# Kernel tuning notes

Hardware: AMD Instinct MI355X
Metric: run time of the kernel (lower is better)

## Reference

```python
import jax, jax.numpy as jnp
import numpy as np

B, L, H = 2, 1024, 1024   # batch, seq_len, hidden_size
NH, D, K = 16, 64, 4      # num_heads, head_dim, conv kernel
HD = NH * D


def setup_inputs() -> dict:
    key = jax.random.key(0)
    ks = jax.random.split(key, 12)
    s = 0.02  # LeCun-ish init scale as in the torch module
    return {
        "hidden_states": jax.random.normal(ks[0], (B, L, H), jnp.float32),
        "Wq": jax.random.normal(ks[1], (HD, H), jnp.float32) * s,
        "bq": jnp.zeros((HD,), jnp.float32),
        "Wk": jax.random.normal(ks[2], (HD, H), jnp.float32) * s,
        "bk": jnp.zeros((HD,), jnp.float32),
        "Wv": jax.random.normal(ks[3], (HD, H), jnp.float32) * s,
        "bv": jnp.zeros((HD,), jnp.float32),
        "Wa": jax.random.normal(ks[4], (NH, H), jnp.float32) * s,
        "Wb": jax.random.normal(ks[5], (NH, H), jnp.float32) * s,
        "Wconv": jax.random.normal(ks[6], (HD, 1, K), jnp.float32) * s,
        "Wo": jax.random.normal(ks[7], (H, HD), jnp.float32) * s,
        "bo": jnp.zeros((H,), jnp.float32),
    }


def _gated_delta(q, k, v, alpha, beta):
    # q,k,v: [B,L,NH,D]; alpha,beta: [B,L,NH]
    # S_t = S_{t-1} @ (alpha_t * (I - beta_t k_t k_t^T)) + beta_t v_t k_t^T ; o_t = S_t q_t
    eye = jnp.eye(q.shape[-1], dtype=q.dtype)

    def step(S, xs):
        q_t, k_t, v_t, a_t, b_t = xs  # [B,NH,D], [B,NH]
        kk = jnp.einsum('bhd,bhe->bhde', k_t, k_t)
        decay = a_t[..., None, None] * (eye - b_t[..., None, None] * kk)
        S = jnp.einsum('bhde,bhef->bhdf', S, decay) \
            + b_t[..., None, None] * jnp.einsum('bhd,bhe->bhde', v_t, k_t)
        o_t = jnp.einsum('bhde,bhe->bhd', S, q_t)
        return S, o_t

    xs = (jnp.moveaxis(q, 1, 0), jnp.moveaxis(k, 1, 0), jnp.moveaxis(v, 1, 0),
          jnp.moveaxis(alpha, 1, 0), jnp.moveaxis(beta, 1, 0))
    S0 = jnp.zeros((q.shape[0], q.shape[2], q.shape[3], q.shape[3]), q.dtype)
    _, outs = jax.lax.scan(step, S0, xs)  # [L,B,NH,D]
    return jnp.transpose(outs, (1, 2, 0, 3))  # [B,NH,L,D] (matches torch stack+transposes)


def reference(hidden_states, Wq, bq, Wk, bk, Wv, bv, Wa, Wb, Wconv, Wo, bo):
    Bc, Lc, Hc = hidden_states.shape
    q = (hidden_states @ Wq.T + bq).reshape(Bc, Lc, NH, D)
    k = (hidden_states @ Wk.T + bk).reshape(Bc, Lc, NH, D)
    v = (hidden_states @ Wv.T + bv).reshape(Bc, Lc, NH, D)
    alpha = jax.nn.sigmoid(hidden_states @ Wa.T)   # [B,L,NH]
    beta = jax.nn.softplus(hidden_states @ Wb.T)   # [B,L,NH]

    out = _gated_delta(q, k, v, alpha, beta)       # [B,NH,L,D]
    out = out.reshape(Bc, Lc, NH * D)              # replicates torch's reshape of [B,NH,L,D]
    x = jnp.transpose(out, (0, 2, 1))              # [B,HD,L]
    conv = jax.lax.conv_general_dilated(
        x, Wconv, window_strides=(1,), padding=[(K - 1, 0)],
        feature_group_count=NH * D, dimension_numbers=('NCH', 'OIH', 'NCH'))
    x = x + conv                                   # residual depthwise causal conv
    x = jnp.transpose(x, (0, 2, 1))                # [B,L,HD]
    return x @ Wo.T + bo                           # [B,L,H]; dropout is identity at eval
```

## Files before the change

kernel.cpp:

```cpp
#include <hip/hip_runtime.h>
#include <math.h>

#define BB 2
#define LL 1024
#define HH 1024
#define NH 16
#define DD 64
#define HD (NH * DD)
#define MM (BB * LL)
#define RCT 32
#define KEXT 3072
#define NBK 1088

typedef _Float16 f16x8 __attribute__((ext_vector_type(8)));
typedef _Float16 f16x4 __attribute__((ext_vector_type(4)));
typedef float f32x4 __attribute__((ext_vector_type(4)));

__device__ __forceinline__ void load_lds16(const void* g, void* l) {
    __builtin_amdgcn_global_load_lds(
        (const __attribute__((address_space(1))) void*)g,
        (__attribute__((address_space(3))) void*)l, 16, 0, 0);
}

__global__ __launch_bounds__(256) void convert_front(
    const float* __restrict__ hs,
    const float* __restrict__ Wq, const float* __restrict__ Wk,
    const float* __restrict__ Wv, const float* __restrict__ Wa,
    const float* __restrict__ Wb, const float* __restrict__ Wo,
    _Float16* __restrict__ Ae3,
    _Float16* __restrict__ Bk, _Float16* __restrict__ Bqv,
    _Float16* __restrict__ Be2)
{
    const int blk = blockIdx.x;
    const int t = threadIdx.x;

    if (blk < 2048) {
        float4 x = *(const float4*)(hs + (size_t)blk * 1024 + t * 4);
        x.x *= 16.f; x.y *= 16.f; x.z *= 16.f; x.w *= 16.f;
        f16x4 h, l;
        h[0] = (_Float16)x.x; l[0] = (_Float16)(x.x - (float)h[0]);
        h[1] = (_Float16)x.y; l[1] = (_Float16)(x.y - (float)h[1]);
        h[2] = (_Float16)x.z; l[2] = (_Float16)(x.z - (float)h[2]);
        h[3] = (_Float16)x.w; l[3] = (_Float16)(x.w - (float)h[3]);
        _Float16* base = Ae3 + (size_t)blk * KEXT + t * 4;
        *(f16x4*)(base)        = h;
        *(f16x4*)(base + 1024) = l;
        *(f16x4*)(base + 2048) = h;
        return;
    }
    if (blk < 3136) {
        const int n = blk - 2048;
        const float* src = nullptr;
        if (n < 1024)      src = Wk + (size_t)n * 1024;
        else if (n < 1040) src = Wa + (size_t)(n - 1024) * 1024;
        else if (n < 1056) src = Wb + (size_t)(n - 1040) * 1024;
        float4 x = src ? *(const float4*)(src + t * 4)
                       : make_float4(0.f, 0.f, 0.f, 0.f);
        x.x *= 64.f; x.y *= 64.f; x.z *= 64.f; x.w *= 64.f;
        f16x4 h, l;
        h[0] = (_Float16)x.x; l[0] = (_Float16)(x.x - (float)h[0]);
        h[1] = (_Float16)x.y; l[1] = (_Float16)(x.y - (float)h[1]);
        h[2] = (_Float16)x.z; l[2] = (_Float16)(x.z - (float)h[2]);
        h[3] = (_Float16)x.w; l[3] = (_Float16)(x.w - (float)h[3]);
        _Float16* base = Bk + (size_t)n * KEXT + t * 4;
        *(f16x4*)(base)        = h;
        *(f16x4*)(base + 1024) = h;
        *(f16x4*)(base + 2048) = l;
        return;
    }
    if (blk < 5184) {
        const int n = blk - 3136;
        const float* src = (n < 1024) ? Wq + (size_t)n * 1024
                                      : Wv + (size_t)(n - 1024) * 1024;
        float4 x = *(const float4*)(src + t * 4);
        f16x4 h;
        h[0] = (_Float16)(x.x * 64.f);
        h[1] = (_Float16)(x.y * 64.f);
        h[2] = (_Float16)(x.z * 64.f);
        h[3] = (_Float16)(x.w * 64.f);
        *(f16x4*)(Bqv + (size_t)n * 1024 + t * 4) = h;
        return;
    }
    {
        const int n = blk - 5184;
        float4 x = *(const float4*)(Wo + (size_t)n * 1024 + t * 4);
        f16x4 h;
        h[0] = (_Float16)(x.x * 64.f);
        h[1] = (_Float16)(x.y * 64.f);
        h[2] = (_Float16)(x.z * 64.f);
        h[3] = (_Float16)(x.w * 64.f);
        *(f16x4*)(Be2 + (size_t)n * 1024 + t * 4) = h;
    }
}

__global__ __launch_bounds__(256) void mfma_gemm_proj(
    const _Float16* __restrict__ Ae3, const _Float16* __restrict__ Bk,
    const _Float16* __restrict__ Bqv,
    float* __restrict__ qkv, float* __restrict__ ab,
    const float* __restrict__ bq, const float* __restrict__ bk,
    const float* __restrict__ bv)
{
    __shared__ __align__(16) _Float16 As[2][128 * 32];
    __shared__ __align__(16) _Float16 Bs[2][128 * 32];

    const int blk = blockIdx.x;
    const int tid = threadIdx.x;
    const int wave = tid >> 6;
    const int lane = tid & 63;
    const int srow = lane >> 2;
    const int scol = (lane & 3) * 8;
    const int fm = lane & 15;
    const int fq = (lane >> 4) * 8;
    const int rquad = (lane >> 4) * 4;

    if (blk < 272) {
        const int bm = (blk / 17) * 128;
        const int bn = (blk % 17) * 64;
        const int wr = (wave >> 1) * 64;
        const int wc = (wave & 1) * 32;

        const _Float16* gA0 = Ae3 + (size_t)(bm + wave * 32 + srow) * KEXT + scol;
        const _Float16* gA1 = gA0 + (size_t)16 * KEXT;
        const _Float16* gB0 = Bk + (size_t)(bn + wave * 16 + srow) * KEXT + scol;
        _Float16* lA0_0 = &As[0][(wave * 32) * 32];
        _Float16* lA1_0 = &As[0][(wave * 32 + 16) * 32];
        _Float16* lB0_0 = &Bs[0][(wave * 16) * 32];
        _Float16* lA0_1 = &As[1][(wave * 32) * 32];
        _Float16* lA1_1 = &As[1][(wave * 32 + 16) * 32];
        _Float16* lB0_1 = &Bs[1][(wave * 16) * 32];

        f32x4 acc[4][2] = {};

        for (int k0 = 0; k0 < KEXT; k0 += 64) {
            load_lds16(gA0 + k0,      lA0_0);
            load_lds16(gA1 + k0,      lA1_0);
            load_lds16(gB0 + k0,      lB0_0);
            load_lds16(gA0 + k0 + 32, lA0_1);
            load_lds16(gA1 + k0 + 32, lA1_1);
            load_lds16(gB0 + k0 + 32, lB0_1);
            __syncthreads();

            #pragma unroll
            for (int s = 0; s < 2; ++s) {
                f16x8 a[4], b[2];
                #pragma unroll
                for (int mt = 0; mt < 4; ++mt)
                    a[mt] = *(const f16x8*)&As[s][(wr + mt * 16 + fm) * 32 + fq];
                #pragma unroll
                for (int nt = 0; nt < 2; ++nt)
                    b[nt] = *(const f16x8*)&Bs[s][(wc + nt * 16 + fm) * 32 + fq];
                #pragma unroll
                for (int mt = 0; mt < 4; ++mt)
                    #pragma unroll
                    for (int nt = 0; nt < 2; ++nt)
                        acc[mt][nt] = __builtin_amdgcn_mfma_f32_16x16x32_f16(
                            a[mt], b[nt], acc[mt][nt], 0, 0, 0);
            }
            __syncthreads();
        }

        #pragma unroll
        for (int mt = 0; mt < 4; ++mt) {
            #pragma unroll
            for (int nt = 0; nt < 2; ++nt) {
                const int col = bn + wc + nt * 16 + fm;
                #pragma unroll
                for (int i = 0; i < 4; ++i) {
                    const int row = bm + wr + mt * 16 + rquad + i;
                    float val = acc[mt][nt][i] * (1.0f / 1024.0f);
                    if (col < 1024)
                        qkv[(size_t)row * 3072 + 1024 + col] = val + bk[col];
                    else if (col < 1040)
                        ab[(size_t)row * 32 + (col - 1024)] =
                            1.f / (1.f + expf(-val));
                    else if (col < 1056)
                        ab[(size_t)row * 32 + 16 + (col - 1040)] =
                            fmaxf(val, 0.f) + log1pf(expf(-fabsf(val)));
                }
            }
        }
    } else {
        const int n = blk - 272;
        const int bm = (n / 16) * 128;
        const int bn = (n % 16) * 128;
        const int wr = (wave >> 1) * 64;
        const int wc = (wave & 1) * 64;

        const _Float16* gA0 = Ae3 + (size_t)(bm + wave * 32 + srow) * KEXT + scol;
        const _Float16* gA1 = gA0 + (size_t)16 * KEXT;
        const _Float16* gB0 = Bqv + (size_t)(bn + wave * 32 + srow) * 1024 + scol;
        const _Float16* gB1 = gB0 + (size_t)16 * 1024;
        _Float16* lA0_0 = &As[0][(wave * 32) * 32];
        _Float16* lA1_0 = &As[0][(wave * 32 + 16) * 32];
        _Float16* lB0_0 = &Bs[0][(wave * 32) * 32];
        _Float16* lB1_0 = &Bs[0][(wave * 32 + 16) * 32];
        _Float16* lA0_1 = &As[1][(wave * 32) * 32];
        _Float16* lA1_1 = &As[1][(wave * 32 + 16) * 32];
        _Float16* lB0_1 = &Bs[1][(wave * 32) * 32];
        _Float16* lB1_1 = &Bs[1][(wave * 32 + 16) * 32];

        f32x4 acc[4][4] = {};

        for (int k0 = 0; k0 < 1024; k0 += 64) {
            load_lds16(gA0 + k0,      lA0_0);
            load_lds16(gA1 + k0,      lA1_0);
            load_lds16(gB0 + k0,      lB0_0);
            load_lds16(gB1 + k0,      lB1_0);
            load_lds16(gA0 + k0 + 32, lA0_1);
            load_lds16(gA1 + k0 + 32, lA1_1);
            load_lds16(gB0 + k0 + 32, lB0_1);
            load_lds16(gB1 + k0 + 32, lB1_1);
            __syncthreads();

            #pragma unroll
            for (int s = 0; s < 2; ++s) {
                f16x8 a[4], b[4];
                #pragma unroll
                for (int mt = 0; mt < 4; ++mt)
                    a[mt] = *(const f16x8*)&As[s][(wr + mt * 16 + fm) * 32 + fq];
                #pragma unroll
                for (int nt = 0; nt < 4; ++nt)
                    b[nt] = *(const f16x8*)&Bs[s][(wc + nt * 16 + fm) * 32 + fq];
                #pragma unroll
                for (int mt = 0; mt < 4; ++mt)
                    #pragma unroll
                    for (int nt = 0; nt < 4; ++nt)
                        acc[mt][nt] = __builtin_amdgcn_mfma_f32_16x16x32_f16(
                            a[mt], b[nt], acc[mt][nt], 0, 0, 0);
            }
            __syncthreads();
        }

        #pragma unroll
        for (int mt = 0; mt < 4; ++mt) {
            #pragma unroll
            for (int nt = 0; nt < 4; ++nt) {
                const int col = bn + wc + nt * 16 + fm;
                #pragma unroll
                for (int i = 0; i < 4; ++i) {
                    const int row = bm + wr + mt * 16 + rquad + i;
                    float val = acc[mt][nt][i] * (1.0f / 1024.0f);
                    if (col < 1024)
                        qkv[(size_t)row * 3072 + col] = val + bq[col];
                    else
                        qkv[(size_t)row * 3072 + 1024 + col] = val + bv[col - 1024];
                }
            }
        }
    }
}

__global__ __launch_bounds__(256) void mfma_gemm_out(
    const _Float16* __restrict__ Ae2, const _Float16* __restrict__ Be2,
    float* __restrict__ outp, const float* __restrict__ bo)
{
    __shared__ __align__(16) _Float16 As[2][128 * 32];
    __shared__ __align__(16) _Float16 Bs[2][64 * 32];

    const int tid = threadIdx.x;
    const int wave = tid >> 6;
    const int lane = tid & 63;
    const int bm = blockIdx.y * 128;
    const int bn = blockIdx.x * 64;
    const int wr = (wave >> 1) * 64;
    const int wc = (wave & 1) * 32;

    const int srow = lane >> 2;
    const int scol = (lane & 3) * 8;
    const _Float16* gA0 = Ae2 + (size_t)(bm + wave * 32 + srow) * 1024 + scol;
    const _Float16* gA1 = gA0 + (size_t)16 * 1024;
    const _Float16* gB0 = Be2 + (size_t)(bn + wave * 16 + srow) * 1024 + scol;
    _Float16* lA0_0 = &As[0][(wave * 32) * 32];
    _Float16* lA1_0 = &As[0][(wave * 32 + 16) * 32];
    _Float16* lB0_0 = &Bs[0][(wave * 16) * 32];
    _Float16* lA0_1 = &As[1][(wave * 32) * 32];
    _Float16* lA1_1 = &As[1][(wave * 32 + 16) * 32];
    _Float16* lB0_1 = &Bs[1][(wave * 16) * 32];

    const int fm = lane & 15;
    const int fq = (lane >> 4) * 8;

    f32x4 acc[4][2] = {};

    for (int k0 = 0; k0 < 1024; k0 += 64) {
        load_lds16(gA0 + k0,      lA0_0);
        load_lds16(gA1 + k0,      lA1_0);
        load_lds16(gB0 + k0,      lB0_0);
        load_lds16(gA0 + k0 + 32, lA0_1);
        load_lds16(gA1 + k0 + 32, lA1_1);
        load_lds16(gB0 + k0 + 32, lB0_1);
        __syncthreads();

        #pragma unroll
        for (int s = 0; s < 2; ++s) {
            f16x8 a[4], b[2];
            #pragma unroll
            for (int mt = 0; mt < 4; ++mt)
                a[mt] = *(const f16x8*)&As[s][(wr + mt * 16 + fm) * 32 + fq];
            #pragma unroll
            for (int nt = 0; nt < 2; ++nt)
                b[nt] = *(const f16x8*)&Bs[s][(wc + nt * 16 + fm) * 32 + fq];
            #pragma unroll
            for (int mt = 0; mt < 4; ++mt)
                #pragma unroll
                for (int nt = 0; nt < 2; ++nt)
                    acc[mt][nt] = __builtin_amdgcn_mfma_f32_16x16x32_f16(
                        a[mt], b[nt], acc[mt][nt], 0, 0, 0);
        }
        __syncthreads();
    }

    const int rquad = (lane >> 4) * 4;
    #pragma unroll
    for (int mt = 0; mt < 4; ++mt) {
        #pragma unroll
        for (int nt = 0; nt < 2; ++nt) {
            const int col = bn + wc + nt * 16 + fm;
            #pragma unroll
            for (int i = 0; i < 4; ++i) {
                const int row = bm + wr + mt * 16 + rquad + i;
                outp[(size_t)row * 1024 + col] = acc[mt][nt][i] * 64.f + bo[col];
            }
        }
    }
}

template <int CTRL>
__device__ __forceinline__ float dpp_addf(float x) {
    int y = __builtin_amdgcn_update_dpp(0, __builtin_bit_cast(int, x),
                                        CTRL, 0xF, 0xF, true);
    return x + __builtin_bit_cast(float, y);
}
__device__ __forceinline__ float red16(float x) {
    x = dpp_addf<0xB1>(x);
    x = dpp_addf<0x4E>(x);
    x = dpp_addf<0x124>(x);
    x = dpp_addf<0x128>(x);
    return x;
}

typedef __attribute__((address_space(3))) const float* lds_cfp;

__device__ __forceinline__ float4 ds_read_f4(lds_cfp p) {
    float4 d;
    asm volatile("ds_read_b128 %0, %1" : "=v"(d) : "v"(p));
    return d;
}

template <int I> struct RdKQ {
    static __device__ __forceinline__ void go(float4* k, float4* q,
                                              lds_cfp kb, lds_cfp qb) {
        k[I] = ds_read_f4(kb + I * 64);
        q[I] = ds_read_f4(qb + I * 64);
        RdKQ<I + 1>::go(k, q, kb, qb);
    }
};
template <> struct RdKQ<16> {
    static __device__ __forceinline__ void go(float4*, float4*, lds_cfp, lds_cfp) {}
};

template <int I> struct RdVAB {
    static __device__ __forceinline__ void go(float4* v, float4* a, float4* b,
                                              lds_cfp vb, lds_cfp abb) {
        v[I] = ds_read_f4(vb + I * 4);
        a[I] = ds_read_f4(abb + I * 4);
        b[I] = ds_read_f4(abb + RCT + I * 4);
        RdVAB<I + 1>::go(v, a, b, vb, abb);
    }
};
template <> struct RdVAB<4> {
    static __device__ __forceinline__ void go(float4*, float4*, float4*, lds_cfp, lds_cfp) {}
};

#define GDN_STEP(T)                                                     \
    {                                                                   \
        const float4 kc = kv[T];                                        \
        const float4 qc = qv[T];                                        \
        const float vc = vv[(T) >> 2][(T) & 3];                         \
        const float ac = av[(T) >> 2][(T) & 3];                         \
        const float bc = bvr[(T) >> 2][(T) & 3];                        \
        float p0 = fmaf(S1, kc.y, S0 * kc.x);                           \
        float p1 = fmaf(S3, kc.w, S2 * kc.z);                           \
        float sk = red16(p0 + p1);                                      \
        const float cf = bc * fmaf(-ac, sk, vc);                        \
        S0 = fmaf(ac, S0, cf * kc.x);                                   \
        S1 = fmaf(ac, S1, cf * kc.y);                                   \
        S2 = fmaf(ac, S2, cf * kc.z);                                   \
        S3 = fmaf(ac, S3, cf * kc.w);                                   \
        float q0 = fmaf(S1, qc.y, S0 * qc.x);                           \
        float q1 = fmaf(S3, qc.w, S2 * qc.z);                           \
        qp[T] = q0 + q1;                                                \
    }

#define GDN_FLUSH(TBASE)                                                \
    {                                                                   \
        _Pragma("unroll")                                               \
        for (int i = 0; i < 16; ++i) qp[i] = dpp_addf<0xB1>(qp[i]);     \
        _Pragma("unroll")                                               \
        for (int i = 0; i < 16; ++i) qp[i] = dpp_addf<0x4E>(qp[i]);     \
        _Pragma("unroll")                                               \
        for (int i = 0; i < 16; ++i) qp[i] = dpp_addf<0x124>(qp[i]);    \
        _Pragma("unroll")                                               \
        for (int i = 0; i < 16; ++i) qp[i] = dpp_addf<0x128>(qp[i]);    \
        if (el == 0) {                                                  \
            *(float4*)(op + (TBASE) + 0)  = make_float4(qp[0],  qp[1],  qp[2],  qp[3]);  \
            *(float4*)(op + (TBASE) + 4)  = make_float4(qp[4],  qp[5],  qp[6],  qp[7]);  \
            *(float4*)(op + (TBASE) + 8)  = make_float4(qp[8],  qp[9],  qp[10], qp[11]); \
            *(float4*)(op + (TBASE) + 12) = make_float4(qp[12], qp[13], qp[14], qp[15]); \
        }                                                               \
    }

__global__ __launch_bounds__(64) void gdn_recurrence(
    const float* __restrict__ qkv, const float* __restrict__ ab,
    float* __restrict__ att)
{
    __shared__ __align__(16) float ks[2][RCT][64];
    __shared__ __align__(16) float qs[2][RCT][64];
    __shared__ __align__(16) float vs_t[2][4][RCT];
    __shared__ __align__(16) float gab_t[2][2][RCT];

    const int blk = blockIdx.x;
    const int bh = blk & 31;
    const int s  = blk >> 5;
    const int b  = bh >> 4;
    const int h  = bh & 15;
    const int lane = threadIdx.x;
    const int rl = lane >> 4;
    const int el = lane & 15;
    const int e0 = el * 4;
    const int r0 = s * 4;

    const float* qb  = qkv + (size_t)b * LL * 3072 + h * 64;
    const float* kb  = qb + 1024;
    const float* vb  = qb + 2048 + r0;
    const float* abp = ab + (size_t)b * LL * 32 + h;
    float* op = att + ((size_t)(b * NH + h) * DD + r0 + rl) * LL;

    const int st = lane >> 4;
    const int sd = (lane & 15) * 4;

    float S0 = 0.f, S1 = 0.f, S2 = 0.f, S3 = 0.f;

    {
        const size_t ro = (size_t)st * 3072 + sd;
        #pragma unroll
        for (int m = 0; m < 8; ++m) {
            load_lds16(kb + ro + (size_t)m * 4 * 3072, &ks[0][m * 4][0]);
            load_lds16(qb + ro + (size_t)m * 4 * 3072, &qs[0][m * 4][0]);
        }
        float4 pv = make_float4(0.f,0.f,0.f,0.f);
        if (lane < RCT) pv = *(const float4*)(vb + (size_t)lane * 3072);
        float pab = (lane < 32) ? abp[(size_t)lane * 32]
                                : abp[(size_t)(lane - 32) * 32 + 16];
        if (lane < RCT) {
            vs_t[0][0][lane] = pv.x;
            vs_t[0][1][lane] = pv.y;
            vs_t[0][2][lane] = pv.z;
            vs_t[0][3][lane] = pv.w;
        }
        if (lane < 32) gab_t[0][0][lane] = pab;
        else           gab_t[0][1][lane - 32] = pab;
    }
    __syncthreads();

    const int NCHUNK = LL / RCT;
    for (int c = 0; c < NCHUNK; ++c) {
        const int cur = c & 1, nxt = cur ^ 1;
        const bool more = (c + 1 < NCHUNK);

        float4 pv = make_float4(0.f,0.f,0.f,0.f);
        float pab = 0.f;
        if (more) {
            const size_t t0 = (size_t)(c + 1) * RCT;
            const size_t ro = (t0 + st) * 3072 + sd;
            #pragma unroll
            for (int m = 0; m < 8; ++m) {
                load_lds16(kb + ro + (size_t)m * 4 * 3072, &ks[nxt][m * 4][0]);
                load_lds16(qb + ro + (size_t)m * 4 * 3072, &qs[nxt][m * 4][0]);
            }
            if (lane < RCT) pv = *(const float4*)(vb + (t0 + lane) * 3072);
            pab = (lane < 32) ? abp[(t0 + lane) * 32]
                              : abp[(t0 + lane - 32) * 32 + 16];
        }

        float4 kv[16], qv[16], vv[4], av[4], bvr[4];
        float qp[16];

        RdKQ<0>::go(kv, qv, (lds_cfp)&ks[cur][0][e0], (lds_cfp)&qs[cur][0][e0]);
        RdVAB<0>::go(vv, av, bvr, (lds_cfp)&vs_t[cur][rl][0],
                     (lds_cfp)&gab_t[cur][0][0]);
        asm volatile("s_waitcnt lgkmcnt(0)" ::: "memory");
        __builtin_amdgcn_sched_barrier(0);
        #pragma unroll
        for (int t = 0; t < 16; ++t) GDN_STEP(t);
        GDN_FLUSH(c * RCT);

        RdKQ<0>::go(kv, qv, (lds_cfp)&ks[cur][16][e0], (lds_cfp)&qs[cur][16][e0]);
        RdVAB<0>::go(vv, av, bvr, (lds_cfp)&vs_t[cur][rl][16],
                     (lds_cfp)&gab_t[cur][0][16]);
        asm volatile("s_waitcnt lgkmcnt(0)" ::: "memory");
        __builtin_amdgcn_sched_barrier(0);
        #pragma unroll
        for (int t = 0; t < 16; ++t) GDN_STEP(t);
        GDN_FLUSH(c * RCT + 16);

        if (more) {
            if (lane < RCT) {
                vs_t[nxt][0][lane] = pv.x;
                vs_t[nxt][1][lane] = pv.y;
                vs_t[nxt][2][lane] = pv.z;
                vs_t[nxt][3][lane] = pv.w;
            }
            if (lane < 32) gab_t[nxt][0][lane] = pab;
            else           gab_t[nxt][1][lane - 32] = pab;
        }
        __syncthreads();
    }
}

__global__ __launch_bounds__(256) void conv_convert(
    const float* __restrict__ att, const float* __restrict__ Wconv,
    _Float16* __restrict__ Ae2)
{
    __shared__ float yt[112][68];
    const int lb = blockIdx.x;
    const int h  = blockIdx.y;
    const int b  = blockIdx.z;
    const int tid = threadIdx.x;

    {
        const int d = tid >> 2;
        const int part = tid & 3;
        const float* src  = att + ((size_t)(b * NH + h) * DD + d) * LL;
        const float* srcm = src - (size_t)DD * LL;
        #pragma unroll
        for (int m = 0; m < 7; ++m) {
            const int off = (part * 7 + m) * 4;
            const int lg = lb * 64 - 48 + off;
            float4 v;
            if (lg >= 0)      v = *(const float4*)(src + lg);
            else if (h > 0)   v = *(const float4*)(srcm + lg + 1024);
            else              v = make_float4(0.f, 0.f, 0.f, 0.f);
            yt[off + 0][d] = v.x; yt[off + 1][d] = v.y;
            yt[off + 2][d] = v.z; yt[off + 3][d] = v.w;
        }
    }
    __syncthreads();

    float4 w[4];
    #pragma unroll
    for (int k = 0; k < 4; ++k)
        w[k] = ((const float4*)Wconv)[tid * 4 + k];

    const int d0 = (tid & 15) * 4;
    const int lq = tid >> 4;
    const float sc = 1.f / 4096.f;

    #pragma unroll
    for (int rr = 0; rr < 4; ++rr) {
        const int ll = rr * 16 + lq;
        float y0[4], y1[4], y2[4], y3[4];
        *(float4*)y0 = *(const float4*)&yt[ll +  0][d0];
        *(float4*)y1 = *(const float4*)&yt[ll + 16][d0];
        *(float4*)y2 = *(const float4*)&yt[ll + 32][d0];
        *(float4*)y3 = *(const float4*)&yt[ll + 48][d0];
        f16x4 hi;
        #pragma unroll
        for (int k = 0; k < 4; ++k) {
            float acc = y3[k];
            acc = fmaf(w[k].x, y0[k], acc);
            acc = fmaf(w[k].y, y1[k], acc);
            acc = fmaf(w[k].z, y2[k], acc);
            acc = fmaf(w[k].w, y3[k], acc);
            hi[k] = (_Float16)(acc * sc);
        }
        const size_t row = (size_t)b * 1024 + h * 64 + lb * 4 + rr;
        *(f16x4*)(Ae2 + row * 1024 + tid * 4) = hi;
    }
}

extern "C" void kernel_launch(void* const* d_in, const int* in_sizes, int n_in,
                              void* d_out, int out_size, void* d_ws, size_t ws_size,
                              hipStream_t stream)
{
    const float* hs    = (const float*)d_in[0];
    const float* Wq    = (const float*)d_in[1];
    const float* bq    = (const float*)d_in[2];
    const float* Wk    = (const float*)d_in[3];
    const float* bk    = (const float*)d_in[4];
    const float* Wv    = (const float*)d_in[5];
    const float* bv    = (const float*)d_in[6];
    const float* Wa    = (const float*)d_in[7];
    const float* Wb    = (const float*)d_in[8];
    const float* Wconv = (const float*)d_in[9];
    const float* Wo    = (const float*)d_in[10];
    const float* bo    = (const float*)d_in[11];
    float* out = (float*)d_out;

    char* w = (char*)d_ws;
    float* qkv = (float*)w;        w += (size_t)MM * 3072 * 4;
    float* att = (float*)w;        w += (size_t)MM * 1024 * 4;
    float* ab  = (float*)w;        w += (size_t)MM * 32 * 4;
    _Float16* Ae3 = (_Float16*)w;  w += (size_t)MM * KEXT * 2;
    _Float16* Bk  = (_Float16*)w;  w += (size_t)NBK * KEXT * 2;
    _Float16* Bqv = (_Float16*)w;  w += (size_t)2048 * 1024 * 2;
    _Float16* Ae2 = (_Float16*)w;  w += (size_t)MM * 1024 * 2;
    _Float16* Be2 = (_Float16*)w;  w += (size_t)1024 * 1024 * 2;

    hipLaunchKernelGGL(convert_front, dim3(6208), dim3(256), 0, stream,
                       hs, Wq, Wk, Wv, Wa, Wb, Wo, Ae3, Bk, Bqv, Be2);

    hipLaunchKernelGGL(mfma_gemm_proj, dim3(528), dim3(256), 0, stream,
                       Ae3, Bk, Bqv, qkv, ab, bq, bk, bv);

    hipLaunchKernelGGL(gdn_recurrence, dim3(512), dim3(64), 0, stream, qkv, ab, att);

    hipLaunchKernelGGL(conv_convert, dim3(16, 16, BB), dim3(256), 0, stream,
                       att, Wconv, Ae2);

    hipLaunchKernelGGL(mfma_gemm_out, dim3(1024 / 64, MM / 128), dim3(256), 0, stream,
                       Ae2, Be2, out, bo);
}
```

Measured before the change: 281.3 us.

## Process recurrence steps in pairs using precomputed k·k and k·q dot products

A new prepass kernel computes, for each pair of consecutive timesteps, the dot products k_t·k_{t+1}, k_t·q_t, k_t·q_{t+1} and k_{t+1}·q_{t+1} per head. The recurrence then advances two timesteps per iteration with a single batched four-way cross-lane reduction, rather than one reduction per step plus a deferred reduction of the outputs. This shortens the serial dependency chain of DPP reductions on the critical path. It costs an extra kernel launch, extra global traffic and LDS staging for the pair scalars, and more FMAs per step.

```diff
diff --git a/kernel.cpp b/kernel.cpp
--- a/kernel.cpp
+++ b/kernel.cpp
@@ -331,12 +331,49 @@
                                         CTRL, 0xF, 0xF, true);
     return x + __builtin_bit_cast(float, y);
 }
-__device__ __forceinline__ float red16(float x) {
-    x = dpp_addf<0xB1>(x);
-    x = dpp_addf<0x4E>(x);
-    x = dpp_addf<0x124>(x);
-    x = dpp_addf<0x128>(x);
-    return x;
+__device__ __forceinline__ void red16x4(float& x0, float& x1,
+                                        float& x2, float& x3) {
+    x0 = dpp_addf<0xB1>(x0);  x1 = dpp_addf<0xB1>(x1);
+    x2 = dpp_addf<0xB1>(x2);  x3 = dpp_addf<0xB1>(x3);
+    x0 = dpp_addf<0x4E>(x0);  x1 = dpp_addf<0x4E>(x1);
+    x2 = dpp_addf<0x4E>(x2);  x3 = dpp_addf<0x4E>(x3);
+    x0 = dpp_addf<0x124>(x0); x1 = dpp_addf<0x124>(x1);
+    x2 = dpp_addf<0x124>(x2); x3 = dpp_addf<0x124>(x3);
+    x0 = dpp_addf<0x128>(x0); x1 = dpp_addf<0x128>(x1);
+    x2 = dpp_addf<0x128>(x2); x3 = dpp_addf<0x128>(x3);
+}
+
+__global__ __launch_bounds__(64) void pair_prepass(
+    const float* __restrict__ qkv, float* __restrict__ Pq)
+{
+    const int blk = blockIdx.x;
+    const int bh = blk >> 5;
+    const int seg = blk & 31;
+    const int b = bh >> 4, h = bh & 15;
+    const int lane = threadIdx.x;
+    const int rl = lane >> 4;
+    const int el = lane & 15;
+    const int e0 = el * 4;
+    const float* qb = qkv + (size_t)b * LL * 3072 + h * 64;
+    const float* kb = qb + 1024;
+
+    #pragma unroll
+    for (int pp_ = 0; pp_ < 4; ++pp_) {
+        const int p = seg * 16 + pp_ * 4 + rl;
+        const int t = 2 * p;
+        const float4 kA = *(const float4*)(kb + (size_t)t * 3072 + e0);
+        const float4 kB = *(const float4*)(kb + (size_t)(t + 1) * 3072 + e0);
+        const float4 qA = *(const float4*)(qb + (size_t)t * 3072 + e0);
+        const float4 qB = *(const float4*)(qb + (size_t)(t + 1) * 3072 + e0);
+        float kk  = fmaf(kA.y, kB.y, kA.x * kB.x) + fmaf(kA.w, kB.w, kA.z * kB.z);
+        float kqA = fmaf(kA.y, qA.y, kA.x * qA.x) + fmaf(kA.w, qA.w, kA.z * qA.z);
+        float kqB = fmaf(kA.y, qB.y, kA.x * qB.x) + fmaf(kA.w, qB.w, kA.z * qB.z);
+        float kqC = fmaf(kB.y, qB.y, kB.x * qB.x) + fmaf(kB.w, qB.w, kB.z * qB.z);
+        red16x4(kk, kqA, kqB, kqC);
+        if (el == 0)
+            *(float4*)(Pq + ((size_t)bh * 512 + p) * 4) =
+                make_float4(kk, kqA, kqB, kqC);
+    }
 }
 
 typedef __attribute__((address_space(3))) const float* lds_cfp;
@@ -372,52 +409,69 @@
     static __device__ __forceinline__ void go(float4*, float4*, float4*, lds_cfp, lds_cfp) {}
 };
 
-#define GDN_STEP(T)                                                     \
+template <int I> struct RdP {
+    static __device__ __forceinline__ void go(float4* p, lds_cfp pb) {
+        p[I] = ds_read_f4(pb + I * 4);
+        RdP<I + 1>::go(p, pb);
+    }
+};
+template <> struct RdP<8> {
+    static __device__ __forceinline__ void go(float4*, lds_cfp) {}
+};
+
+#define GDN_PAIR(P)                                                     \
     {                                                                   \
-        const float4 kc = kv[T];                                        \
-        const float4 qc = qv[T];                                        \
-        const float vc = vv[(T) >> 2][(T) & 3];                         \
-        const float ac = av[(T) >> 2][(T) & 3];                         \
-        const float bc = bvr[(T) >> 2][(T) & 3];                        \
-        float p0 = fmaf(S1, kc.y, S0 * kc.x);                           \
-        float p1 = fmaf(S3, kc.w, S2 * kc.z);                           \
-        float sk = red16(p0 + p1);                                      \
-        const float cf = bc * fmaf(-ac, sk, vc);                        \
-        S0 = fmaf(ac, S0, cf * kc.x);                                   \
-        S1 = fmaf(ac, S1, cf * kc.y);                                   \
-        S2 = fmaf(ac, S2, cf * kc.z);                                   \
-        S3 = fmaf(ac, S3, cf * kc.w);                                   \
-        float q0 = fmaf(S1, qc.y, S0 * qc.x);                           \
-        float q1 = fmaf(S3, qc.w, S2 * qc.z);                           \
-        qp[T] = q0 + q1;                                                \
-    }
-
-#define GDN_FLUSH(TBASE)                                                \
-    {                                                                   \
-        _Pragma("unroll")                                               \
-        for (int i = 0; i < 16; ++i) qp[i] = dpp_addf<0xB1>(qp[i]);     \
-        _Pragma("unroll")                                               \
-        for (int i = 0; i < 16; ++i) qp[i] = dpp_addf<0x4E>(qp[i]);     \
-        _Pragma("unroll")                                               \
-        for (int i = 0; i < 16; ++i) qp[i] = dpp_addf<0x124>(qp[i]);    \
-        _Pragma("unroll")                                               \
-        for (int i = 0; i < 16; ++i) qp[i] = dpp_addf<0x128>(qp[i]);    \
-        if (el == 0) {                                                  \
-            *(float4*)(op + (TBASE) + 0)  = make_float4(qp[0],  qp[1],  qp[2],  qp[3]);  \
-            *(float4*)(op + (TBASE) + 4)  = make_float4(qp[4],  qp[5],  qp[6],  qp[7]);  \
-            *(float4*)(op + (TBASE) + 8)  = make_float4(qp[8],  qp[9],  qp[10], qp[11]); \
-            *(float4*)(op + (TBASE) + 12) = make_float4(qp[12], qp[13], qp[14], qp[15]); \
-        }                                                               \
+        const float4 k1 = kv[2 * (P)];                                  \
+        const float4 k2 = kv[2 * (P) + 1];                              \
+        const float4 q1 = qv[2 * (P)];                                  \
+        const float4 q2 = qv[2 * (P) + 1];                              \
+        const float v1 = vv[(P) >> 1][(2 * (P)) & 3];                   \
+        const float v2 = vv[(P) >> 1][(2 * (P) + 1) & 3];               \
+        const float a1 = av[(P) >> 1][(2 * (P)) & 3];                   \
+        const float a2 = av[(P) >> 1][(2 * (P) + 1) & 3];               \
+        const float b1 = bvr[(P) >> 1][(2 * (P)) & 3];                  \
+        const float b2 = bvr[(P) >> 1][(2 * (P) + 1) & 3];              \
+        const float4 pp = pv4[P];                                       \
+        float skA = fmaf(S1, k1.y, S0 * k1.x) + fmaf(S3, k1.w, S2 * k1.z); \
+        float skB = fmaf(S1, k2.y, S0 * k2.x) + fmaf(S3, k2.w, S2 * k2.z); \
+        float sqA = fmaf(S1, q1.y, S0 * q1.x) + fmaf(S3, q1.w, S2 * q1.z); \
+        float sqB = fmaf(S1, q2.y, S0 * q2.x) + fmaf(S3, q2.w, S2 * q2.z); \
+        const float aS0 = a1 * S0, aS1 = a1 * S1;                       \
+        const float aS2 = a1 * S2, aS3 = a1 * S3;                       \
+        red16x4(skA, skB, sqA, sqB);                                    \
+        const float cf = b1 * fmaf(-a1, skA, v1);                       \
+        const float sk2 = fmaf(cf, pp.x, a1 * skB);                     \
+        const float cf2 = b2 * fmaf(-a2, sk2, v2);                      \
+        const float T0 = fmaf(cf, k1.x, aS0);                           \
+        const float T1 = fmaf(cf, k1.y, aS1);                           \
+        const float T2 = fmaf(cf, k1.z, aS2);                           \
+        const float T3 = fmaf(cf, k1.w, aS3);                           \
+        S0 = fmaf(cf2, k2.x, a2 * T0);                                  \
+        S1 = fmaf(cf2, k2.y, a2 * T1);                                  \
+        S2 = fmaf(cf2, k2.z, a2 * T2);                                  \
+        S3 = fmaf(cf2, k2.w, a2 * T3);                                  \
+        qp[2 * (P)] = fmaf(cf, pp.y, a1 * sqA);                         \
+        const float inn = fmaf(cf, pp.z, a1 * sqB);                     \
+        qp[2 * (P) + 1] = fmaf(cf2, pp.w, a2 * inn);                    \
+    }
+
+#define GDN_STORE(TBASE)                                                \
+    if (el == 0) {                                                      \
+        *(float4*)(op + (TBASE) + 0)  = make_float4(qp[0],  qp[1],  qp[2],  qp[3]);  \
+        *(float4*)(op + (TBASE) + 4)  = make_float4(qp[4],  qp[5],  qp[6],  qp[7]);  \
+        *(float4*)(op + (TBASE) + 8)  = make_float4(qp[8],  qp[9],  qp[10], qp[11]); \
+        *(float4*)(op + (TBASE) + 12) = make_float4(qp[12], qp[13], qp[14], qp[15]); \
     }
 
 __global__ __launch_bounds__(64) void gdn_recurrence(
     const float* __restrict__ qkv, const float* __restrict__ ab,
-    float* __restrict__ att)
+    const float* __restrict__ Pq, float* __restrict__ att)
 {
     __shared__ __align__(16) float ks[2][RCT][64];
     __shared__ __align__(16) float qs[2][RCT][64];
     __shared__ __align__(16) float vs_t[2][4][RCT];
     __shared__ __align__(16) float gab_t[2][2][RCT];
+    __shared__ __align__(16) float ps[2][16][4];
 
     const int blk = blockIdx.x;
     const int bh = blk & 31;
@@ -434,6 +488,7 @@
     const float* kb  = qb + 1024;
     const float* vb  = qb + 2048 + r0;
     const float* abp = ab + (size_t)b * LL * 32 + h;
+    const float* Pg  = Pq + (size_t)bh * 512 * 4;
     float* op = att + ((size_t)(b * NH + h) * DD + r0 + rl) * LL;
 
     const int st = lane >> 4;
@@ -448,6 +503,7 @@
             load_lds16(kb + ro + (size_t)m * 4 * 3072, &ks[0][m * 4][0]);
             load_lds16(qb + ro + (size_t)m * 4 * 3072, &qs[0][m * 4][0]);
         }
+        if (lane < 16) load_lds16(Pg + (size_t)lane * 4, &ps[0][0][0]);
         float4 pv = make_float4(0.f,0.f,0.f,0.f);
         if (lane < RCT) pv = *(const float4*)(vb + (size_t)lane * 3072);
         float pab = (lane < 32) ? abp[(size_t)lane * 32]
@@ -478,31 +534,36 @@
                 load_lds16(kb + ro + (size_t)m * 4 * 3072, &ks[nxt][m * 4][0]);
                 load_lds16(qb + ro + (size_t)m * 4 * 3072, &qs[nxt][m * 4][0]);
             }
+            if (lane < 16)
+                load_lds16(Pg + (size_t)((c + 1) * 16 + lane) * 4,
+                           &ps[nxt][0][0]);
             if (lane < RCT) pv = *(const float4*)(vb + (t0 + lane) * 3072);
             pab = (lane < 32) ? abp[(t0 + lane) * 32]
                               : abp[(t0 + lane - 32) * 32 + 16];
         }
 
-        float4 kv[16], qv[16], vv[4], av[4], bvr[4];
+        float4 kv[16], qv[16], vv[4], av[4], bvr[4], pv4[8];
         float qp[16];
 
         RdKQ<0>::go(kv, qv, (lds_cfp)&ks[cur][0][e0], (lds_cfp)&qs[cur][0][e0]);
         RdVAB<0>::go(vv, av, bvr, (lds_cfp)&vs_t[cur][rl][0],
                      (lds_cfp)&gab_t[cur][0][0]);
+        RdP<0>::go(pv4, (lds_cfp)&ps[cur][0][0]);
         asm volatile("s_waitcnt lgkmcnt(0)" ::: "memory");
         __builtin_amdgcn_sched_barrier(0);
-        #pragma unroll
-        for (int t = 0; t < 16; ++t) GDN_STEP(t);
-        GDN_FLUSH(c * RCT);
+        GDN_PAIR(0) GDN_PAIR(1) GDN_PAIR(2) GDN_PAIR(3)
+        GDN_PAIR(4) GDN_PAIR(5) GDN_PAIR(6) GDN_PAIR(7)
+        GDN_STORE(c * RCT);
 
         RdKQ<0>::go(kv, qv, (lds_cfp)&ks[cur][16][e0], (lds_cfp)&qs[cur][16][e0]);
         RdVAB<0>::go(vv, av, bvr, (lds_cfp)&vs_t[cur][rl][16],
                      (lds_cfp)&gab_t[cur][0][16]);
+        RdP<0>::go(pv4, (lds_cfp)&ps[cur][8][0]);
         asm volatile("s_waitcnt lgkmcnt(0)" ::: "memory");
         __builtin_amdgcn_sched_barrier(0);
-        #pragma unroll
-        for (int t = 0; t < 16; ++t) GDN_STEP(t);
-        GDN_FLUSH(c * RCT + 16);
+        GDN_PAIR(0) GDN_PAIR(1) GDN_PAIR(2) GDN_PAIR(3)
+        GDN_PAIR(4) GDN_PAIR(5) GDN_PAIR(6) GDN_PAIR(7)
+        GDN_STORE(c * RCT + 16);
 
         if (more) {
             if (lane < RCT) {
@@ -606,6 +667,7 @@
     _Float16* Bqv = (_Float16*)w;  w += (size_t)2048 * 1024 * 2;
     _Float16* Ae2 = (_Float16*)w;  w += (size_t)MM * 1024 * 2;
     _Float16* Be2 = (_Float16*)w;  w += (size_t)1024 * 1024 * 2;
+    float* Pq  = (float*)w;        w += (size_t)32 * 512 * 4 * 4;
 
     hipLaunchKernelGGL(convert_front, dim3(6208), dim3(256), 0, stream,
                        hs, Wq, Wk, Wv, Wa, Wb, Wo, Ae3, Bk, Bqv, Be2);
@@ -613,7 +675,10 @@
     hipLaunchKernelGGL(mfma_gemm_proj, dim3(528), dim3(256), 0, stream,
                        Ae3, Bk, Bqv, qkv, ab, bq, bk, bv);
 
-    hipLaunchKernelGGL(gdn_recurrence, dim3(512), dim3(64), 0, stream, qkv, ab, att);
+    hipLaunchKernelGGL(pair_prepass, dim3(1024), dim3(64), 0, stream, qkv, Pq);
+
+    hipLaunchKernelGGL(gdn_recurrence, dim3(512), dim3(64), 0, stream,
+                       qkv, ab, Pq, att);
 
     hipLaunchKernelGGL(conv_convert, dim3(16, 16, BB), dim3(256), 0, stream,
                        att, Wconv, Ae2);
```

After: 280.6 us, median of 3. No clear change (-0.3%).
